# Performance work log

Hardware: AMD Instinct MI355X
Metric: run time of the kernel (lower is better)

The kernel has to match this reference:

```python
import jax, jax.numpy as jnp
import numpy as np

N = 100000   # real nodes
E = 100000   # real edges (tree-like rumor cascades)
B = 128      # graphs in batch
IN = 256     # in_feats
HID = 128    # GCN hidden
OUT = 128    # out_feats


def setup_inputs() -> dict:
    key = jax.random.key(0)
    ks = jax.random.split(key, 16)
    sc = lambda k, sh: (jax.random.normal(k, sh, jnp.float32) * 0.05)
    x = jax.random.normal(ks[0], (N, IN), jnp.float32)
    edge_index = jax.random.randint(ks[1], (2, E), 0, N, jnp.int32)
    # sorted segment ids, every graph non-empty (equal split)
    batch = ((jnp.arange(N, dtype=jnp.int32) * B) // N).astype(jnp.int32)
    return {
        "x": x,
        "emb_w": sc(ks[2], (1, IN)),
        "td_w1": sc(ks[3], (IN, HID)), "td_b1": sc(ks[4], (HID,)),
        "td_w2": sc(ks[5], (HID, OUT)), "td_b2": sc(ks[6], (OUT,)),
        "bu_w1": sc(ks[7], (IN, HID)), "bu_b1": sc(ks[8], (HID,)),
        "bu_w2": sc(ks[9], (HID, OUT)), "bu_b2": sc(ks[10], (OUT,)),
        "p_w1": sc(ks[11], (2 * OUT, 256)), "p_b1": sc(ks[12], (256,)),
        "p_w2": sc(ks[13], (256, 128)), "p_b2": sc(ks[14], (128,)),
        "edge_index": edge_index,
        "batch": batch,
        "num_graphs": B,
    }


def gcn_conv(h, src, dst, W, b, n):
    # PyG GCNConv: transform, add self-loops, symmetric normalization, scatter-add
    h = h @ W
    loops = jnp.arange(n, dtype=src.dtype)
    s = jnp.concatenate([src, loops])
    d = jnp.concatenate([dst, loops])
    deg = jax.ops.segment_sum(jnp.ones(s.shape, h.dtype), d, num_segments=n)
    dinv = jax.lax.rsqrt(deg)  # deg >= 1 thanks to self-loops
    norm = dinv[s] * dinv[d]
    out = jax.ops.segment_sum(h[s] * norm[:, None], d, num_segments=n)
    return out + b


def reference(x, emb_w, td_w1, td_b1, td_w2, td_b2,
              bu_w1, bu_b1, bu_w2, bu_b2,
              p_w1, p_b1, p_w2, p_b2,
              edge_index, batch, num_graphs):
    n = x.shape[0]
    nv = n + 1  # with virtual node
    xv = jnp.concatenate([x, emb_w], axis=0)
    # root = first node of each graph (batch is sorted)
    roots = jnp.searchsorted(batch, jnp.arange(num_graphs, dtype=batch.dtype)).astype(edge_index.dtype)
    vsrc = jnp.full((num_graphs,), n, edge_index.dtype)
    src = jnp.concatenate([edge_index[0], vsrc])
    dst = jnp.concatenate([edge_index[1], roots])

    def branch(s, d, w1, b1, w2, b2):
        h = jax.nn.relu(gcn_conv(xv, s, d, w1, b1, nv))
        # dropout is identity in eval mode
        h = gcn_conv(h, s, d, w2, b2, nv)
        # Prompt=True: pool real nodes, add virtual-node embedding
        return jax.ops.segment_sum(h[:-1], batch, num_segments=num_graphs) + h[-1]

    td = branch(src, dst, td_w1, td_b1, td_w2, td_b2)
    bu = branch(dst, src, bu_w1, bu_b1, bu_w2, bu_b2)  # flipped edges
    h = jnp.concatenate([bu, td], axis=1)  # [B, 2*OUT]
    return jax.nn.relu(h @ p_w1 + p_b1) @ p_w2 + p_b2  # [B, 128]
```

## Files before the change

kernel.cpp:

```cpp
#include <hip/hip_runtime.h>

typedef __bf16 bf16_t;
typedef __bf16 bf16x8 __attribute__((ext_vector_type(8)));
typedef float f32x4 __attribute__((ext_vector_type(4)));

#define INF 256
#define HF 128
#define NPB 16
#define SLMASK 0x00FFFFFF
#define SCAN_STRIDE 512

__device__ inline float2 bf2_to_f2(unsigned v) {
    float lo = __uint_as_float(v << 16);
    float hi = __uint_as_float(v & 0xffff0000u);
    return make_float2(lo, hi);
}
__device__ inline unsigned f2_to_bf2(float a, float b) {
    __bf16 x = (__bf16)a, y = (__bf16)b;
    unsigned short ux = __builtin_bit_cast(unsigned short, x);
    unsigned short uy = __builtin_bit_cast(unsigned short, y);
    return (unsigned)ux | ((unsigned)uy << 16);
}

__global__ void k_roots(const int* __restrict__ batch, int* __restrict__ roots, int N, int B) {
    int i = blockIdx.x * blockDim.x + threadIdx.x;
    if (i == 0) roots[B] = N;
    if (i < N) {
        if (i == 0) roots[batch[0]] = 0;
        else if (batch[i] != batch[i - 1]) roots[batch[i]] = i;
    }
}

__global__ void k_zero(int* __restrict__ p, int n) {
    int i = blockIdx.x * blockDim.x + threadIdx.x;
    if (i < n) p[i] = 0;
}

__global__ void k_wswz2(const float* __restrict__ tw1, const float* __restrict__ bw1,
                        bf16_t* __restrict__ o) {
    int idx = blockIdx.x * blockDim.x + threadIdx.x;
    if (idx >= 65536) return;
    const float* W = (idx < 32768) ? tw1 : bw1;
    bf16_t* out = o + (idx & 32768);
    int i = idx & 32767;
    int j  = i & 7;
    int l  = (i >> 3) & 63;
    int t  = i >> 9;
    int n  = t & 7;
    int kk = t >> 3;
    int k  = kk * 32 + ((l >> 4) << 3) + j;
    int c  = (n << 4) + (l & 15);
    out[i] = (bf16_t)W[k * HF + c];
}

__global__ void k_degboth(const int* __restrict__ src, const int* __restrict__ dst,
                          const int* __restrict__ roots, int* __restrict__ indeg,
                          int E, int B, int N, int nv) {
    int e = blockIdx.x * blockDim.x + threadIdx.x;
    if (e >= E + B) return;
    int a, b;
    if (e < E) { a = src[e]; b = dst[e]; }
    else       { a = N;      b = roots[e - E]; }
    atomicAdd(&indeg[b], 1);
    atomicAdd(&indeg[nv + a], 1);
}

__global__ void k_dinvboth(const int* __restrict__ indeg, float* __restrict__ dinv, int n2) {
    int i = blockIdx.x * blockDim.x + threadIdx.x;
    if (i < n2) dinv[i] = rsqrtf(1.0f + (float)indeg[i]);
}

__global__ __launch_bounds__(256) void k_scan1(const int* __restrict__ indeg, int* __restrict__ bsum, int nv) {
    int dir = blockIdx.y;
    __shared__ int s[256];
    int t = threadIdx.x;
    int v = blockIdx.x * 256 + t;
    s[t] = (v < nv) ? indeg[dir * nv + v] : 0;
    __syncthreads();
    for (int off = 128; off > 0; off >>= 1) {
        if (t < off) s[t] += s[t + off];
        __syncthreads();
    }
    if (t == 0) bsum[dir * SCAN_STRIDE + blockIdx.x] = s[0];
}

__global__ __launch_bounds__(512) void k_scan2(int* __restrict__ bsum, int nblk) {
    int dir = blockIdx.y;
    int* p = bsum + dir * SCAN_STRIDE;
    __shared__ int s[512];
    int t = threadIdx.x;
    int v = (t < nblk) ? p[t] : 0;
    s[t] = v;
    __syncthreads();
    for (int off = 1; off < 512; off <<= 1) {
        int u = (t >= off) ? s[t - off] : 0;
        __syncthreads();
        s[t] += u;
        __syncthreads();
    }
    if (t < nblk) p[t] = s[t] - v;
}

__global__ __launch_bounds__(256) void k_scan3(const int* __restrict__ indeg, const int* __restrict__ bsum,
                                               int* __restrict__ off, int* __restrict__ cursor,
                                               int nv, int total) {
    int dir = blockIdx.y;
    __shared__ int s[256];
    int t = threadIdx.x;
    int v0 = blockIdx.x * 256 + t;
    int val = (v0 < nv) ? indeg[dir * nv + v0] : 0;
    s[t] = val;
    __syncthreads();
    for (int o = 1; o < 256; o <<= 1) {
        int u = (t >= o) ? s[t - o] : 0;
        __syncthreads();
        s[t] += u;
        __syncthreads();
    }
    int excl = s[t] - val + bsum[dir * SCAN_STRIDE + blockIdx.x];
    if (v0 < nv) {
        off[dir * (nv + 1) + v0] = excl;
        cursor[dir * nv + v0] = excl;
    }
    if (blockIdx.x == 0 && t == 0) off[dir * (nv + 1) + nv] = total;
}

__global__ void k_fill(const int* __restrict__ src, const int* __restrict__ dst,
                       const int* __restrict__ roots, int* __restrict__ cursor,
                       int* __restrict__ slots,
                       int E, int B, int N, int nv) {
    int e = blockIdx.x * blockDim.x + threadIdx.x;
    if (e >= E + B) return;
    int EB = E + B;
    int a, b;
    if (e < E) { a = src[e]; b = dst[e]; }
    else       { a = N;      b = roots[e - E]; }
    int p = atomicAdd(&cursor[b], 1);
    slots[p] = a | ((b & (NPB - 1)) << 24);
    p = atomicAdd(&cursor[nv + a], 1);
    slots[EB + p] = b | ((a & (NPB - 1)) << 24);
}

__global__ __launch_bounds__(256) void k_gemm1both(
    const float* __restrict__ x, const float* __restrict__ emb,
    const bf16_t* __restrict__ WfTD, const bf16_t* __restrict__ WfBU,
    const float* __restrict__ dinvTD, const float* __restrict__ dinvBU,
    bf16_t* __restrict__ rawsTD, bf16_t* __restrict__ rawsBU,
    int nv, int N)
{
    int lane = threadIdx.x & 63;
    int wave = threadIdx.x >> 6;
    int rowbase = blockIdx.x * 64 + wave * 16;
    int r = rowbase + (lane & 15);
    int kseg = lane >> 4;
    const float* xr = (r < N) ? (x + (size_t)r * INF) : emb;

    bf16x8 a[8];
    #pragma unroll
    for (int h = 0; h < 2; ++h) {
        float4 f[8];
        #pragma unroll
        for (int kk = 0; kk < 4; ++kk) {
            int k0 = (h * 4 + kk) * 32 + kseg * 8;
            f[2 * kk]     = *reinterpret_cast<const float4*>(xr + k0);
            f[2 * kk + 1] = *reinterpret_cast<const float4*>(xr + k0 + 4);
        }
        #pragma unroll
        for (int kk = 0; kk < 4; ++kk) {
            bf16x8 av;
            av[0] = (__bf16)f[2 * kk].x;     av[1] = (__bf16)f[2 * kk].y;
            av[2] = (__bf16)f[2 * kk].z;     av[3] = (__bf16)f[2 * kk].w;
            av[4] = (__bf16)f[2 * kk + 1].x; av[5] = (__bf16)f[2 * kk + 1].y;
            av[6] = (__bf16)f[2 * kk + 1].z; av[7] = (__bf16)f[2 * kk + 1].w;
            a[h * 4 + kk] = av;
        }
    }

    f32x4 accT[8] = {}, accB[8] = {};
    #pragma unroll
    for (int kk = 0; kk < 8; ++kk) {
        #pragma unroll
        for (int n = 0; n < 8; ++n) {
            size_t wi = (size_t)((((kk << 3) + n) << 6) + lane) * 8;
            bf16x8 bt = *reinterpret_cast<const bf16x8*>(WfTD + wi);
            accT[n] = __builtin_amdgcn_mfma_f32_16x16x32_bf16(a[kk], bt, accT[n], 0, 0, 0);
            bf16x8 bb = *reinterpret_cast<const bf16x8*>(WfBU + wi);
            accB[n] = __builtin_amdgcn_mfma_f32_16x16x32_bf16(a[kk], bb, accB[n], 0, 0, 0);
        }
    }

    int ccol = lane & 15;
    int cg = lane >> 4;
    #pragma unroll
    for (int i = 0; i < 4; ++i) {
        int rr = rowbase + cg * 4 + i;
        if (rr >= nv) continue;
        float diT = dinvTD[rr], diB = dinvBU[rr];
        bf16_t* oT = rawsTD + (size_t)rr * HF + ccol;
        bf16_t* oB = rawsBU + (size_t)rr * HF + ccol;
        #pragma unroll
        for (int n = 0; n < 8; ++n) {
            oT[n * 16] = (bf16_t)(accT[n][i] * diT);
            oB[n * 16] = (bf16_t)(accB[n][i] * diB);
        }
    }
}

__global__ __launch_bounds__(128) void k_gather1(
    const bf16_t* __restrict__ raws, const int* __restrict__ off,
    const int* __restrict__ slots,
    const float* __restrict__ dinv,
    const float* __restrict__ td_b1, const float* __restrict__ bu_b1,
    bf16_t* __restrict__ ab, int nv, int EB)
{
    int dir = blockIdx.y;
    const bf16_t* R  = raws + (size_t)dir * nv * HF;
    const int*    OF = off + (size_t)dir * (nv + 1);
    const int*    SL = slots + (size_t)dir * EB;
    const float*  DV = dinv + (size_t)dir * nv;
    const float*  bias = dir ? bu_b1 : td_b1;
    bf16_t* AB = ab + (size_t)dir * nv * HF;

    __shared__ float2 buf[2][NPB][64];
    int t = threadIdx.x;
    int h = t >> 6;
    int c = t & 63;
    int v0 = blockIdx.x * NPB;

    unsigned selfw[8];
    #pragma unroll
    for (int jj = 0; jj < 8; ++jj) {
        int v = min(v0 + 2 * jj + h, nv - 1);
        selfw[jj] = *reinterpret_cast<const unsigned*>(R + (size_t)v * HF + 2 * c);
    }
    __builtin_amdgcn_sched_barrier(0);
    #pragma unroll
    for (int jj = 0; jj < 8; ++jj) {
        float2 f = bf2_to_f2(selfw[jj]);
        buf[h][2 * jj + h][c] = f;
        buf[h][2 * jj + (1 - h)][c] = make_float2(0.f, 0.f);
    }

    int e0 = OF[v0], e1 = OF[min(v0 + NPB, nv)];
    #pragma unroll 1
    for (int i = e0; i < e1; i += 16) {
        int w[8];
        #pragma unroll
        for (int u = 0; u < 8; ++u) w[u] = SL[min(i + 2 * u + h, e1 - 1)];
        __builtin_amdgcn_sched_barrier(0);
        unsigned vw[8];
        #pragma unroll
        for (int u = 0; u < 8; ++u)
            vw[u] = *reinterpret_cast<const unsigned*>(R + (size_t)(w[u] & SLMASK) * HF + 2 * c);
        __builtin_amdgcn_sched_barrier(0);
        #pragma unroll
        for (int u = 0; u < 8; ++u) {
            if (i + 2 * u + h < e1) {
                float2 f = bf2_to_f2(vw[u]);
                int j = w[u] >> 24;
                float2 cur = buf[h][j][c];
                buf[h][j][c] = make_float2(cur.x + f.x, cur.y + f.y);
            }
        }
    }
    __syncthreads();

    float bs0 = bias[2 * c], bs1 = bias[2 * c + 1];
    #pragma unroll 1
    for (int jj = 0; jj < 8; ++jj) {
        int j = 2 * jj + h;
        int v = v0 + j;
        if (v >= nv) break;
        float2 a0 = buf[0][j][c], a1 = buf[1][j][c];
        float dv = DV[v];
        float x0 = dv * (a0.x + a1.x) + bs0;
        float x1 = dv * (a0.y + a1.y) + bs1;
        unsigned o = f2_to_bf2(dv * fmaxf(x0, 0.f), dv * fmaxf(x1, 0.f));
        *reinterpret_cast<unsigned*>(AB + (size_t)v * HF + 2 * c) = o;
    }
}

__global__ __launch_bounds__(128) void k_gather2pool(
    const bf16_t* __restrict__ ab, const int* __restrict__ off,
    const int* __restrict__ slots,
    const float* __restrict__ dinv, const int* __restrict__ batch,
    float* __restrict__ pooled, float* __restrict__ vrow,
    int nv, int EB, int N, int B)
{
    int dir = blockIdx.y;
    const bf16_t* S  = ab + (size_t)dir * nv * HF;
    const int*    OF = off + (size_t)dir * (nv + 1);
    const int*    SL = slots + (size_t)dir * EB;
    const float*  DV = dinv + (size_t)dir * nv;
    float* PP = pooled + (size_t)dir * B * HF;
    float* VR = vrow + dir * HF;

    __shared__ float2 buf[2][NPB][64];
    int t = threadIdx.x;
    int h = t >> 6;
    int c = t & 63;
    int v0 = blockIdx.x * NPB;

    unsigned selfw[8];
    #pragma unroll
    for (int jj = 0; jj < 8; ++jj) {
        int v = min(v0 + 2 * jj + h, nv - 1);
        selfw[jj] = *reinterpret_cast<const unsigned*>(S + (size_t)v * HF + 2 * c);
    }
    __builtin_amdgcn_sched_barrier(0);
    #pragma unroll
    for (int jj = 0; jj < 8; ++jj) {
        float2 f = bf2_to_f2(selfw[jj]);
        buf[h][2 * jj + h][c] = f;
        buf[h][2 * jj + (1 - h)][c] = make_float2(0.f, 0.f);
    }

    int e0 = OF[v0], e1 = OF[min(v0 + NPB, nv)];
    #pragma unroll 1
    for (int i = e0; i < e1; i += 16) {
        int w[8];
        #pragma unroll
        for (int u = 0; u < 8; ++u) w[u] = SL[min(i + 2 * u + h, e1 - 1)];
        __builtin_amdgcn_sched_barrier(0);
        unsigned vw[8];
        #pragma unroll
        for (int u = 0; u < 8; ++u)
            vw[u] = *reinterpret_cast<const unsigned*>(S + (size_t)(w[u] & SLMASK) * HF + 2 * c);
        __builtin_amdgcn_sched_barrier(0);
        #pragma unroll
        for (int u = 0; u < 8; ++u) {
            if (i + 2 * u + h < e1) {
                float2 f = bf2_to_f2(vw[u]);
                int j = w[u] >> 24;
                float2 cur = buf[h][j][c];
                buf[h][j][c] = make_float2(cur.x + f.x, cur.y + f.y);
            }
        }
    }
    __syncthreads();

    float acc0 = 0.f, acc1 = 0.f;
    int curg = -1;
    #pragma unroll 1
    for (int jj = 0; jj < 8; ++jj) {
        int j = 2 * jj + h;
        int v = v0 + j;
        if (v >= nv) break;
        float2 a0 = buf[0][j][c], a1 = buf[1][j][c];
        float dv = DV[v];
        float G0 = dv * (a0.x + a1.x);
        float G1 = dv * (a0.y + a1.y);
        if (v == N) { VR[2 * c] = G0; VR[2 * c + 1] = G1; continue; }
        int g = batch[v];
        if (g != curg) {
            if (curg >= 0) {
                atomicAdd(&PP[curg * HF + 2 * c], acc0);
                atomicAdd(&PP[curg * HF + 2 * c + 1], acc1);
            }
            curg = g; acc0 = 0.f; acc1 = 0.f;
        }
        acc0 += G0; acc1 += G1;
    }
    if (curg >= 0) {
        atomicAdd(&PP[curg * HF + 2 * c], acc0);
        atomicAdd(&PP[curg * HF + 2 * c + 1], acc1);
    }
}

__global__ __launch_bounds__(256) void k_mlp(
    const float* __restrict__ pooled, const float* __restrict__ vrow, const int* __restrict__ roots,
    const float* __restrict__ td_w2, const float* __restrict__ td_b2,
    const float* __restrict__ bu_w2, const float* __restrict__ bu_b2,
    const float* __restrict__ w1, const float* __restrict__ b1,
    const float* __restrict__ w2, const float* __restrict__ b2,
    float* __restrict__ out, int B)
{
    __shared__ float zsh[256];
    __shared__ float invec[256];
    __shared__ float hid[256];
    int g = blockIdx.x;
    int t = threadIdx.x;
    const float* pp_td = pooled;
    const float* pp_bu = pooled + (size_t)B * HF;
    const float* vr_td = vrow;
    const float* vr_bu = vrow + HF;
    zsh[t] = (t < 128) ? (pp_bu[g * HF + t] + vr_bu[t])
                       : (pp_td[g * HF + (t - 128)] + vr_td[t - 128]);
    __syncthreads();
    float cnt1 = (float)(roots[g + 1] - roots[g] + 1);
    float acc2;
    if (t < 128) {
        acc2 = cnt1 * bu_b2[t];
        #pragma unroll 8
        for (int k = 0; k < 128; ++k) acc2 = fmaf(zsh[k], bu_w2[k * HF + t], acc2);
    } else {
        int tt = t - 128;
        acc2 = cnt1 * td_b2[tt];
        #pragma unroll 8
        for (int k = 0; k < 128; ++k) acc2 = fmaf(zsh[128 + k], td_w2[k * HF + tt], acc2);
    }
    invec[t] = acc2;
    __syncthreads();
    float acc = b1[t];
    #pragma unroll 8
    for (int k = 0; k < 256; ++k) acc = fmaf(invec[k], w1[k * 256 + t], acc);
    hid[t] = acc > 0.f ? acc : 0.f;
    __syncthreads();
    if (t < 128) {
        float o = b2[t];
        #pragma unroll 8
        for (int k = 0; k < 256; ++k) o = fmaf(hid[k], w2[k * 128 + t], o);
        out[g * 128 + t] = o;
    }
}

extern "C" void kernel_launch(void* const* d_in, const int* in_sizes, int n_in,
                              void* d_out, int out_size, void* d_ws, size_t ws_size,
                              hipStream_t stream) {
    const float* x     = (const float*)d_in[0];
    const float* emb_w = (const float*)d_in[1];
    const float* td_w1 = (const float*)d_in[2];
    const float* td_b1 = (const float*)d_in[3];
    const float* td_w2 = (const float*)d_in[4];
    const float* td_b2 = (const float*)d_in[5];
    const float* bu_w1 = (const float*)d_in[6];
    const float* bu_b1 = (const float*)d_in[7];
    const float* bu_w2 = (const float*)d_in[8];
    const float* bu_b2 = (const float*)d_in[9];
    const float* p_w1  = (const float*)d_in[10];
    const float* p_b1  = (const float*)d_in[11];
    const float* p_w2  = (const float*)d_in[12];
    const float* p_b2  = (const float*)d_in[13];
    const int*   ei    = (const int*)d_in[14];
    const int*   batch = (const int*)d_in[15];

    int N = in_sizes[0] / INF;
    int E = in_sizes[14] / 2;
    int B = out_size / 128;
    int nv = N + 1;
    int EB = E + B;
    const int* src = ei;
    const int* dst = ei + E;

    char* wsp = (char*)d_ws;
    auto alloc = [&](size_t bytes) { char* p = wsp; wsp += (bytes + 255) & ~(size_t)255; return p; };
    int zwords = 2 * nv + 2 * B * HF + 2 * HF;
    int*    Z      = (int*)   alloc((size_t)zwords * 4);
    int*    indeg  = Z;
    float*  pooled = (float*)(Z + 2 * nv);
    float*  vrow   = pooled + 2 * B * HF;
    float*  dinv   = (float*) alloc((size_t)2 * nv * 4);
    int*    off    = (int*)   alloc((size_t)2 * (nv + 1) * 4);
    int*    cursor = (int*)   alloc((size_t)2 * nv * 4);
    int*    slots  = (int*)   alloc((size_t)2 * EB * 4);
    int*    bsum   = (int*)   alloc((size_t)2 * SCAN_STRIDE * 4);
    int*    roots  = (int*)   alloc((size_t)(B + 1) * 4);
    bf16_t* Wf     = (bf16_t*)alloc((size_t)65536 * 2);
    bf16_t* RAWS   = (bf16_t*)alloc((size_t)2 * nv * HF * 2);
    bf16_t* AB     = (bf16_t*)alloc((size_t)2 * nv * HF * 2);

    float* out = (float*)d_out;

    dim3 b256(256), b128(128);
    int nblk = (nv + 255) / 256;
    int ngb = (nv + NPB - 1) / NPB;
    int nvb = (nv + 63) / 64;

    k_roots<<<dim3((N + 255) / 256), b256, 0, stream>>>(batch, roots, N, B);
    k_zero<<<dim3((zwords + 255) / 256), b256, 0, stream>>>(Z, zwords);
    k_wswz2<<<dim3((65536 + 255) / 256), b256, 0, stream>>>(td_w1, bu_w1, Wf);
    k_degboth<<<dim3((EB + 255) / 256), b256, 0, stream>>>(src, dst, roots, indeg, E, B, N, nv);
    k_dinvboth<<<dim3((2 * nv + 255) / 256), b256, 0, stream>>>(indeg, dinv, 2 * nv);
    k_scan1<<<dim3(nblk, 2), b256, 0, stream>>>(indeg, bsum, nv);
    k_scan2<<<dim3(1, 2), dim3(512), 0, stream>>>(bsum, nblk);
    k_scan3<<<dim3(nblk, 2), b256, 0, stream>>>(indeg, bsum, off, cursor, nv, EB);
    k_fill<<<dim3((EB + 255) / 256), b256, 0, stream>>>(src, dst, roots, cursor, slots, E, B, N, nv);

    k_gemm1both<<<dim3(nvb), b256, 0, stream>>>(
        x, emb_w, Wf, Wf + 32768, dinv, dinv + nv,
        RAWS, RAWS + (size_t)nv * HF, nv, N);

    k_gather1<<<dim3(ngb, 2), b128, 0, stream>>>(
        RAWS, off, slots, dinv, td_b1, bu_b1, AB, nv, EB);

    k_gather2pool<<<dim3(ngb, 2), b128, 0, stream>>>(
        AB, off, slots, dinv, batch, pooled, vrow, nv, EB, N, B);

    k_mlp<<<dim3(B), b256, 0, stream>>>(
        pooled, vrow, roots, td_w2, td_b2, bu_w2, bu_b2,
        p_w1, p_b1, p_w2, p_b2, out, B);
}
```

Baseline: 228.9 us.

## Stage GEMM weights in LDS and use register accumulators in gathers

The first-layer GEMM now copies each k-slice of both weight matrices into shared memory with block-wide syncs, so the four waves read weights from LDS instead of each fetching them from global memory. Both gather kernels change from a two-half-block LDS accumulation to one wave per 16-node group. Each wave keeps its 16 accumulators in registers and picks the target slot with a readfirstlane plus a switch, which removes LDS traffic and the block barrier. The costs are extra syncs in the GEMM loop, higher register pressure, and serial edge processing within each wave.

```diff
diff --git a/kernel.cpp b/kernel.cpp
--- a/kernel.cpp
+++ b/kernel.cpp
@@ -6,7 +6,7 @@
 
 #define INF 256
 #define HF 128
-#define NPB 16
+#define GRP 16
 #define SLMASK 0x00FFFFFF
 #define SCAN_STRIDE 512
 
@@ -136,9 +136,9 @@
     if (e < E) { a = src[e]; b = dst[e]; }
     else       { a = N;      b = roots[e - E]; }
     int p = atomicAdd(&cursor[b], 1);
-    slots[p] = a | ((b & (NPB - 1)) << 24);
+    slots[p] = a | ((b & (GRP - 1)) << 24);
     p = atomicAdd(&cursor[nv + a], 1);
-    slots[EB + p] = b | ((a & (NPB - 1)) << 24);
+    slots[EB + p] = b | ((a & (GRP - 1)) << 24);
 }
 
 __global__ __launch_bounds__(256) void k_gemm1both(
@@ -148,12 +148,24 @@
     bf16_t* __restrict__ rawsTD, bf16_t* __restrict__ rawsBU,
     int nv, int N)
 {
+    __shared__ bf16_t WS[8192];
     int lane = threadIdx.x & 63;
     int wave = threadIdx.x >> 6;
     int rowbase = blockIdx.x * 64 + wave * 16;
     int r = rowbase + (lane & 15);
     int kseg = lane >> 4;
     const float* xr = (r < N) ? (x + (size_t)r * INF) : emb;
+
+    auto stage = [&](int kk) {
+        #pragma unroll
+        for (int q = 0; q < 4; ++q) {
+            int idx = q * 256 + threadIdx.x;
+            int d = idx >> 9, r9 = idx & 511;
+            const bf16_t* Wsrc = d ? WfBU : WfTD;
+            *reinterpret_cast<float4*>(WS + (size_t)idx * 8) =
+                *reinterpret_cast<const float4*>(Wsrc + ((size_t)(kk << 9) + r9) * 8);
+        }
+    };
 
     bf16x8 a[8];
     #pragma unroll
@@ -179,14 +191,16 @@
     f32x4 accT[8] = {}, accB[8] = {};
     #pragma unroll
     for (int kk = 0; kk < 8; ++kk) {
+        stage(kk);
+        __syncthreads();
         #pragma unroll
         for (int n = 0; n < 8; ++n) {
-            size_t wi = (size_t)((((kk << 3) + n) << 6) + lane) * 8;
-            bf16x8 bt = *reinterpret_cast<const bf16x8*>(WfTD + wi);
+            bf16x8 bt = *reinterpret_cast<const bf16x8*>(WS + (size_t)(((n << 6) + lane)) * 8);
             accT[n] = __builtin_amdgcn_mfma_f32_16x16x32_bf16(a[kk], bt, accT[n], 0, 0, 0);
-            bf16x8 bb = *reinterpret_cast<const bf16x8*>(WfBU + wi);
+            bf16x8 bb = *reinterpret_cast<const bf16x8*>(WS + 4096 + (size_t)(((n << 6) + lane)) * 8);
             accB[n] = __builtin_amdgcn_mfma_f32_16x16x32_bf16(a[kk], bb, accB[n], 0, 0, 0);
         }
+        if (kk < 7) __syncthreads();
     }
 
     int ccol = lane & 15;
@@ -206,12 +220,18 @@
     }
 }
 
-__global__ __launch_bounds__(128) void k_gather1(
+#define ACC_CASE(K) case K: acc[K].x += f.x; acc[K].y += f.y; break;
+#define ACC_SWITCH(js)  switch (js) { \
+    ACC_CASE(0)  ACC_CASE(1)  ACC_CASE(2)  ACC_CASE(3) \
+    ACC_CASE(4)  ACC_CASE(5)  ACC_CASE(6)  ACC_CASE(7) \
+    ACC_CASE(8)  ACC_CASE(9)  ACC_CASE(10) ACC_CASE(11) \
+    ACC_CASE(12) ACC_CASE(13) ACC_CASE(14) ACC_CASE(15) }
+
+__global__ __launch_bounds__(256) void k_gather1(
     const bf16_t* __restrict__ raws, const int* __restrict__ off,
-    const int* __restrict__ slots,
-    const float* __restrict__ dinv,
+    const int* __restrict__ slots, const float* __restrict__ dinv,
     const float* __restrict__ td_b1, const float* __restrict__ bu_b1,
-    bf16_t* __restrict__ ab, int nv, int EB)
+    bf16_t* __restrict__ ab, int nv, int EB, int N)
 {
     int dir = blockIdx.y;
     const bf16_t* R  = raws + (size_t)dir * nv * HF;
@@ -221,69 +241,65 @@
     const float*  bias = dir ? bu_b1 : td_b1;
     bf16_t* AB = ab + (size_t)dir * nv * HF;
 
-    __shared__ float2 buf[2][NPB][64];
-    int t = threadIdx.x;
-    int h = t >> 6;
-    int c = t & 63;
-    int v0 = blockIdx.x * NPB;
-
-    unsigned selfw[8];
-    #pragma unroll
-    for (int jj = 0; jj < 8; ++jj) {
-        int v = min(v0 + 2 * jj + h, nv - 1);
-        selfw[jj] = *reinterpret_cast<const unsigned*>(R + (size_t)v * HF + 2 * c);
+    int wave = threadIdx.x >> 6;
+    int lane = threadIdx.x & 63;
+    int v0 = (blockIdx.x * 4 + wave) * GRP;
+    if (v0 >= nv) return;
+    int vmax = min(v0 + GRP, nv);
+    int c2 = 2 * lane;
+
+    unsigned selfw[GRP];
+    float dvv[GRP];
+    #pragma unroll
+    for (int j = 0; j < GRP; ++j) {
+        int v = min(v0 + j, nv - 1);
+        selfw[j] = *reinterpret_cast<const unsigned*>(R + (size_t)v * HF + c2);
+        dvv[j] = DV[v];
     }
     __builtin_amdgcn_sched_barrier(0);
-    #pragma unroll
-    for (int jj = 0; jj < 8; ++jj) {
-        float2 f = bf2_to_f2(selfw[jj]);
-        buf[h][2 * jj + h][c] = f;
-        buf[h][2 * jj + (1 - h)][c] = make_float2(0.f, 0.f);
-    }
-
-    int e0 = OF[v0], e1 = OF[min(v0 + NPB, nv)];
+    float2 acc[GRP];
+    #pragma unroll
+    for (int j = 0; j < GRP; ++j) acc[j] = bf2_to_f2(selfw[j]);
+
+    int e0 = OF[v0], e1 = OF[vmax];
     #pragma unroll 1
-    for (int i = e0; i < e1; i += 16) {
+    for (int i = e0; i < e1; i += 8) {
         int w[8];
         #pragma unroll
-        for (int u = 0; u < 8; ++u) w[u] = SL[min(i + 2 * u + h, e1 - 1)];
+        for (int u = 0; u < 8; ++u) w[u] = SL[min(i + u, e1 - 1)];
         __builtin_amdgcn_sched_barrier(0);
         unsigned vw[8];
         #pragma unroll
         for (int u = 0; u < 8; ++u)
-            vw[u] = *reinterpret_cast<const unsigned*>(R + (size_t)(w[u] & SLMASK) * HF + 2 * c);
+            vw[u] = *reinterpret_cast<const unsigned*>(R + (size_t)(w[u] & SLMASK) * HF + c2);
         __builtin_amdgcn_sched_barrier(0);
         #pragma unroll
         for (int u = 0; u < 8; ++u) {
-            if (i + 2 * u + h < e1) {
+            if (i + u < e1) {
                 float2 f = bf2_to_f2(vw[u]);
-                int j = w[u] >> 24;
-                float2 cur = buf[h][j][c];
-                buf[h][j][c] = make_float2(cur.x + f.x, cur.y + f.y);
+                int js = __builtin_amdgcn_readfirstlane(w[u] >> 24);
+                ACC_SWITCH(js)
             }
         }
     }
-    __syncthreads();
-
-    float bs0 = bias[2 * c], bs1 = bias[2 * c + 1];
-    #pragma unroll 1
-    for (int jj = 0; jj < 8; ++jj) {
-        int j = 2 * jj + h;
+
+    float bs0 = bias[c2], bs1 = bias[c2 + 1];
+    #pragma unroll
+    for (int j = 0; j < GRP; ++j) {
         int v = v0 + j;
         if (v >= nv) break;
-        float2 a0 = buf[0][j][c], a1 = buf[1][j][c];
-        float dv = DV[v];
-        float x0 = dv * (a0.x + a1.x) + bs0;
-        float x1 = dv * (a0.y + a1.y) + bs1;
+        float dv = dvv[j];
+        float x0 = fmaf(dv, acc[j].x, bs0);
+        float x1 = fmaf(dv, acc[j].y, bs1);
         unsigned o = f2_to_bf2(dv * fmaxf(x0, 0.f), dv * fmaxf(x1, 0.f));
-        *reinterpret_cast<unsigned*>(AB + (size_t)v * HF + 2 * c) = o;
-    }
-}
-
-__global__ __launch_bounds__(128) void k_gather2pool(
+        *reinterpret_cast<unsigned*>(AB + (size_t)v * HF + c2) = o;
+    }
+}
+
+__global__ __launch_bounds__(256) void k_gather2pool(
     const bf16_t* __restrict__ ab, const int* __restrict__ off,
-    const int* __restrict__ slots,
-    const float* __restrict__ dinv, const int* __restrict__ batch,
+    const int* __restrict__ slots, const float* __restrict__ dinv,
+    const int* __restrict__ batch,
     float* __restrict__ pooled, float* __restrict__ vrow,
     int nv, int EB, int N, int B)
 {
@@ -295,75 +311,72 @@
     float* PP = pooled + (size_t)dir * B * HF;
     float* VR = vrow + dir * HF;
 
-    __shared__ float2 buf[2][NPB][64];
-    int t = threadIdx.x;
-    int h = t >> 6;
-    int c = t & 63;
-    int v0 = blockIdx.x * NPB;
-
-    unsigned selfw[8];
-    #pragma unroll
-    for (int jj = 0; jj < 8; ++jj) {
-        int v = min(v0 + 2 * jj + h, nv - 1);
-        selfw[jj] = *reinterpret_cast<const unsigned*>(S + (size_t)v * HF + 2 * c);
+    int wave = threadIdx.x >> 6;
+    int lane = threadIdx.x & 63;
+    int v0 = (blockIdx.x * 4 + wave) * GRP;
+    if (v0 >= nv) return;
+    int vmax = min(v0 + GRP, nv);
+    int c2 = 2 * lane;
+
+    unsigned selfw[GRP];
+    float dvv[GRP];
+    int bv[GRP];
+    #pragma unroll
+    for (int j = 0; j < GRP; ++j) {
+        int v = min(v0 + j, nv - 1);
+        selfw[j] = *reinterpret_cast<const unsigned*>(S + (size_t)v * HF + c2);
+        dvv[j] = DV[v];
+        bv[j] = batch[min(v, N - 1)];
     }
     __builtin_amdgcn_sched_barrier(0);
-    #pragma unroll
-    for (int jj = 0; jj < 8; ++jj) {
-        float2 f = bf2_to_f2(selfw[jj]);
-        buf[h][2 * jj + h][c] = f;
-        buf[h][2 * jj + (1 - h)][c] = make_float2(0.f, 0.f);
-    }
-
-    int e0 = OF[v0], e1 = OF[min(v0 + NPB, nv)];
+    float2 acc[GRP];
+    #pragma unroll
+    for (int j = 0; j < GRP; ++j) acc[j] = bf2_to_f2(selfw[j]);
+
+    int e0 = OF[v0], e1 = OF[vmax];
     #pragma unroll 1
-    for (int i = e0; i < e1; i += 16) {
+    for (int i = e0; i < e1; i += 8) {
         int w[8];
         #pragma unroll
-        for (int u = 0; u < 8; ++u) w[u] = SL[min(i + 2 * u + h, e1 - 1)];
+        for (int u = 0; u < 8; ++u) w[u] = SL[min(i + u, e1 - 1)];
         __builtin_amdgcn_sched_barrier(0);
         unsigned vw[8];
         #pragma unroll
         for (int u = 0; u < 8; ++u)
-            vw[u] = *reinterpret_cast<const unsigned*>(S + (size_t)(w[u] & SLMASK) * HF + 2 * c);
+            vw[u] = *reinterpret_cast<const unsigned*>(S + (size_t)(w[u] & SLMASK) * HF + c2);
         __builtin_amdgcn_sched_barrier(0);
         #pragma unroll
         for (int u = 0; u < 8; ++u) {
-            if (i + 2 * u + h < e1) {
+            if (i + u < e1) {
                 float2 f = bf2_to_f2(vw[u]);
-                int j = w[u] >> 24;
-                float2 cur = buf[h][j][c];
-                buf[h][j][c] = make_float2(cur.x + f.x, cur.y + f.y);
+                int js = __builtin_amdgcn_readfirstlane(w[u] >> 24);
+                ACC_SWITCH(js)
             }
         }
     }
-    __syncthreads();
-
-    float acc0 = 0.f, acc1 = 0.f;
+
+    float a0 = 0.f, a1 = 0.f;
     int curg = -1;
-    #pragma unroll 1
-    for (int jj = 0; jj < 8; ++jj) {
-        int j = 2 * jj + h;
+    #pragma unroll
+    for (int j = 0; j < GRP; ++j) {
         int v = v0 + j;
         if (v >= nv) break;
-        float2 a0 = buf[0][j][c], a1 = buf[1][j][c];
-        float dv = DV[v];
-        float G0 = dv * (a0.x + a1.x);
-        float G1 = dv * (a0.y + a1.y);
-        if (v == N) { VR[2 * c] = G0; VR[2 * c + 1] = G1; continue; }
-        int g = batch[v];
+        float dv = dvv[j];
+        float G0 = dv * acc[j].x, G1 = dv * acc[j].y;
+        if (v == N) { VR[c2] = G0; VR[c2 + 1] = G1; continue; }
+        int g = bv[j];
         if (g != curg) {
             if (curg >= 0) {
-                atomicAdd(&PP[curg * HF + 2 * c], acc0);
-                atomicAdd(&PP[curg * HF + 2 * c + 1], acc1);
+                atomicAdd(&PP[curg * HF + c2], a0);
+                atomicAdd(&PP[curg * HF + c2 + 1], a1);
             }
-            curg = g; acc0 = 0.f; acc1 = 0.f;
-        }
-        acc0 += G0; acc1 += G1;
+            curg = g; a0 = 0.f; a1 = 0.f;
+        }
+        a0 += G0; a1 += G1;
     }
     if (curg >= 0) {
-        atomicAdd(&PP[curg * HF + 2 * c], acc0);
-        atomicAdd(&PP[curg * HF + 2 * c + 1], acc1);
+        atomicAdd(&PP[curg * HF + c2], a0);
+        atomicAdd(&PP[curg * HF + c2 + 1], a1);
     }
 }
 
@@ -463,7 +476,7 @@
 
     dim3 b256(256), b128(128);
     int nblk = (nv + 255) / 256;
-    int ngb = (nv + NPB - 1) / NPB;
+    int ngb = (nv + 4 * GRP - 1) / (4 * GRP);
     int nvb = (nv + 63) / 64;
 
     k_roots<<<dim3((N + 255) / 256), b256, 0, stream>>>(batch, roots, N, B);
@@ -480,10 +493,10 @@
         x, emb_w, Wf, Wf + 32768, dinv, dinv + nv,
         RAWS, RAWS + (size_t)nv * HF, nv, N);
 
-    k_gather1<<<dim3(ngb, 2), b128, 0, stream>>>(
-        RAWS, off, slots, dinv, td_b1, bu_b1, AB, nv, EB);
-
-    k_gather2pool<<<dim3(ngb, 2), b128, 0, stream>>>(
+    k_gather1<<<dim3(ngb, 2), b256, 0, stream>>>(
+        RAWS, off, slots, dinv, td_b1, bu_b1, AB, nv, EB, N);
+
+    k_gather2pool<<<dim3(ngb, 2), b256, 0, stream>>>(
         AB, off, slots, dinv, batch, pooled, vrow, nv, EB, N, B);
 
     k_mlp<<<dim3(B), b256, 0, stream>>>(
```

New measurement: 261.0 us. 1.14x slower.
